# Kernel tuning notes

Measured on AMD Instinct MI355X. Metric: run time of the kernel, lower is better.

The kernel has to match this reference:

```python
import jax, jax.numpy as jnp
import numpy as np

B, L, D_MODEL = 2, 4096, 1024
D_INNER = 2048  # expand * d_model
D_CONV = 4


def setup_inputs() -> dict:
    key = jax.random.key(0)
    ks = jax.random.split(key, 7)
    return {
        "hidden_states": jax.random.normal(ks[0], (B, L, D_MODEL), jnp.float32),
        "W_in": jax.random.normal(ks[1], (2 * D_INNER, D_MODEL), jnp.float32) * 0.02,
        "conv_w": jax.random.normal(ks[2], (D_INNER, D_CONV), jnp.float32) * 0.1,
        "conv_b": jax.random.normal(ks[3], (D_INNER,), jnp.float32) * 0.1,
        "k_ssm": jax.random.normal(ks[4], (D_INNER, L), jnp.float32) * 0.02,  # materialized SSM kernel (channels=1)
        "D_skip": jax.random.normal(ks[5], (D_INNER,), jnp.float32),
        "W_out": jax.random.normal(ks[6], (D_MODEL, D_INNER), jnp.float32) * 0.02,
    }


def _silu(x):
    return x * jax.nn.sigmoid(x)


def reference(hidden_states, W_in, conv_w, conv_b, k_ssm, D_skip, W_out):
    Bq, Lq, _ = hidden_states.shape
    # in_proj (no bias): (B, L, d_model) -> (B, 2*d_inner, L)
    xz = jnp.einsum('bld,ed->bel', hidden_states, W_in)
    x, z = jnp.split(xz, 2, axis=1)  # each (B, d_inner, L)

    # causal depthwise conv1d (pad left d_conv-1) + SiLU (causal_conv1d_fn)
    xp = jnp.pad(x, ((0, 0), (0, 0), (D_CONV - 1, 0)))
    xc = conv_b[None, :, None]
    for j in range(D_CONV):
        xc = xc + conv_w[None, :, j, None] * xp[:, :, j:j + Lq]
    x = _silu(xc)

    # FFT long convolution (l_kernel = L, n = 2L), channels = 1
    n = 2 * Lq
    x_f = jnp.fft.rfft(x, n=n)            # (B, H, n//2+1) complex
    k_f = jnp.fft.rfft(k_ssm, n=n)        # (H, n//2+1)
    y = jnp.fft.irfft(x_f * k_f[None], n=n)[..., :Lq]  # (B, H, L)

    # D skip connection
    y = y + x * D_skip[None, :, None]

    # gating with SiLU(z)
    y = y * _silu(z)

    # out_proj (no bias): (B, H, L) -> (B, L, d_model)
    return jnp.einsum('bhl,dh->bld', y, W_out)
```

## Files before the change

kernel.cpp:

```cpp
#include <hip/hip_runtime.h>
#include <hip/hip_bf16.h>
#include <math.h>

#define B_SZ 2
#define L_SZ 4096
#define DM   1024
#define DI   2048
#define E_SZ 4096
#define DC   4

typedef unsigned short u16;
typedef __attribute__((ext_vector_type(8))) short short8;
typedef __attribute__((ext_vector_type(4))) float f32x4;

__device__ __forceinline__ float silu_f(float v) {
    return v / (1.0f + __expf(-v));
}

__device__ __forceinline__ void split_bf16(float x, u16& h, u16& l) {
    unsigned u  = __float_as_uint(x);
    unsigned hb = u & 0xFFFF0000u;
    h = (u16)(hb >> 16);
    float lf = x - __uint_as_float(hb);
    l = (u16)(__float_as_uint(lf) >> 16);
}
__device__ __forceinline__ float bf2f(u16 h) {
    return __uint_as_float(((unsigned)h) << 16);
}

__device__ __forceinline__ void gld_lds16(const u16* g, u16* l) {
    __builtin_amdgcn_global_load_lds(
        (const __attribute__((address_space(1))) unsigned int*)g,
        (__attribute__((address_space(3))) unsigned int*)l, 16, 0, 0);
}

__global__ __launch_bounds__(256) void pack_rm(
    const float* __restrict__ X, u16* __restrict__ H, u16* __restrict__ Lo,
    int ldx, int r16n, long sX, long sOut)
{
    const long cid = (long)blockIdx.x * 256 + threadIdx.x;
    const int  qc  = (int)(cid & 63);
    const long blk = cid >> 6;
    const int  r16 = (int)(blk % r16n);
    const int  k32 = (int)(blk / r16n);
    const int  q = qc >> 4, m = qc & 15;

    const float* src = X + blockIdx.y * sX + (long)(r16 * 16 + m) * ldx + k32 * 32 + q * 8;
    float4 v0 = *(const float4*)src;
    float4 v1 = *(const float4*)(src + 4);
    float v[8] = {v0.x,v0.y,v0.z,v0.w,v1.x,v1.y,v1.z,v1.w};

    u16 hs[8], ls[8];
    #pragma unroll
    for (int j = 0; j < 8; ++j) split_bf16(v[j], hs[j], ls[j]);

    const long o = blockIdx.y * sOut + cid * 8;
    *(uint4*)&H[o]  = *(const uint4*)hs;
    *(uint4*)&Lo[o] = *(const uint4*)ls;
}

__global__ __launch_bounds__(256) void gemm_mfma(
    const u16* __restrict__ Ah, const u16* __restrict__ Al,
    const u16* __restrict__ Bh, const u16* __restrict__ Bl,
    float* __restrict__ C,
    int r16A, int r16B, long sA, long sB, long sC,
    int ldc, int nk32)
{
    __shared__ alignas(16) u16 sm[4][4096];

    const int tid  = threadIdx.x;
    const int wv   = tid >> 6, lane = tid & 63;
    const long zb  = blockIdx.z;

    const u16* srcs0 = Ah + zb * sA;
    const u16* srcs1 = Al + zb * sA;
    const u16* srcs2 = Bh + zb * sB;
    const u16* srcs3 = Bl + zb * sB;
    const u16* mysrc = (wv == 0) ? srcs0 : (wv == 1) ? srcs1 : (wv == 2) ? srcs2 : srcs3;
    const int  rblk  = (wv < 2) ? blockIdx.x * 8 : blockIdx.y * 8;
    const int  r16c  = (wv < 2) ? r16A : r16B;
    u16* myl = sm[wv];

    const int wr = wv >> 1, wc = wv & 1;

    f32x4 acc[4][4];
    #pragma unroll
    for (int i = 0; i < 4; ++i)
        #pragma unroll
        for (int j = 0; j < 4; ++j)
            #pragma unroll
            for (int r = 0; r < 4; ++r) acc[i][j][r] = 0.f;

    for (int s = 0; s < nk32; ++s) {
        if (s) __syncthreads();
        {
            const u16* g = mysrc + (((long)s * r16c + rblk) << 9) + lane * 8;
            #pragma unroll
            for (int i = 0; i < 8; ++i)
                gld_lds16(g + (i << 9), myl + (i << 9));
        }
        __syncthreads();

        short8 afh[4], afl[4], bfh[4], bfl[4];
        const int aoff = (wr * 4) * 512 + lane * 8;
        const int boff = (wc * 4) * 512 + lane * 8;
        #pragma unroll
        for (int t = 0; t < 4; ++t) {
            afh[t] = *(const short8*)&sm[0][aoff + t * 512];
            afl[t] = *(const short8*)&sm[1][aoff + t * 512];
            bfh[t] = *(const short8*)&sm[2][boff + t * 512];
            bfl[t] = *(const short8*)&sm[3][boff + t * 512];
        }
        #pragma unroll
        for (int i = 0; i < 4; ++i)
            #pragma unroll
            for (int j = 0; j < 4; ++j) {
                acc[i][j] = __builtin_amdgcn_mfma_f32_16x16x32_bf16(afh[i], bfh[j], acc[i][j], 0, 0, 0);
                acc[i][j] = __builtin_amdgcn_mfma_f32_16x16x32_bf16(afh[i], bfl[j], acc[i][j], 0, 0, 0);
                acc[i][j] = __builtin_amdgcn_mfma_f32_16x16x32_bf16(afl[i], bfh[j], acc[i][j], 0, 0, 0);
            }
    }

    const int m_ = lane & 15, q_ = lane >> 4;
    float* Cb = C + zb * sC;
    const int row00 = blockIdx.x * 128 + wr * 64 + q_ * 4;
    const int col0  = blockIdx.y * 128 + wc * 64 + m_;
    #pragma unroll
    for (int i = 0; i < 4; ++i)
        #pragma unroll
        for (int j = 0; j < 4; ++j) {
            const long base = (long)(row00 + i * 16) * ldc + col0 + j * 16;
            #pragma unroll
            for (int r = 0; r < 4; ++r)
                Cb[base + (long)r * ldc] = acc[i][j][r];
        }
}

__global__ __launch_bounds__(256) void conv_silu_split(
    const float* __restrict__ xz, const float* __restrict__ conv_w,
    const float* __restrict__ conv_b,
    u16* __restrict__ xh_gl, u16* __restrict__ xl_gl)
{
    const long gid = (long)blockIdx.x * 256 + threadIdx.x;
    const int  q   = (int)(gid % (L_SZ / 4));
    const long bc  = gid / (L_SZ / 4);
    const int  ch  = (int)(bc % DI);
    const int  b   = (int)(bc / DI);

    const float* row = xz + ((long)b * E_SZ + ch) * L_SZ;
    const int l0 = q * 4;

    float4 cur  = *(const float4*)&row[l0];
    float4 prev = q ? *(const float4*)&row[l0 - 4] : make_float4(0.f, 0.f, 0.f, 0.f);

    const float w0 = conv_w[ch*DC+0], w1 = conv_w[ch*DC+1];
    const float w2 = conv_w[ch*DC+2], w3 = conv_w[ch*DC+3];
    const float bias = conv_b[ch];

    float o[4];
    o[0] = silu_f(bias + w0*prev.y + w1*prev.z + w2*prev.w + w3*cur.x);
    o[1] = silu_f(bias + w0*prev.z + w1*prev.w + w2*cur.x  + w3*cur.y);
    o[2] = silu_f(bias + w0*prev.w + w1*cur.x  + w2*cur.y  + w3*cur.z);
    o[3] = silu_f(bias + w0*cur.x  + w1*cur.y  + w2*cur.z  + w3*cur.w);

    unsigned long long hp = 0ull, lp = 0ull;
    #pragma unroll
    for (int r = 0; r < 4; ++r) {
        u16 h, l; split_bf16(o[r], h, l);
        hp |= ((unsigned long long)h) << (16*r);
        lp |= ((unsigned long long)l) << (16*r);
    }
    const long base = ((long)b * DI + ch) * L_SZ + l0;
    *(unsigned long long*)&xh_gl[base] = hp;
    *(unsigned long long*)&xl_gl[base] = lp;
}

__global__ __launch_bounds__(128, 2) void longconv_mfma(
    u16* __restrict__ xh_gl, u16* __restrict__ xl_gl,
    const float* __restrict__ xz,  const float* __restrict__ k_ssm,
    const float* __restrict__ D_skip)
{
    __shared__ u16 Xh[2][4352];
    __shared__ u16 Xl[2][4352];

    const int lane = threadIdx.x & 63;
    const int wv   = threadIdx.x >> 6;
    const int wc   = blockIdx.x * 2 + wv;
    const int ch   = wc & (DI - 1);
    const int b    = wc >> 11;

    u16*         xhr  = xh_gl + ((long)b * DI + ch) * L_SZ;
    u16*         xlr  = xl_gl + ((long)b * DI + ch) * L_SZ;
    const float* krow = k_ssm + (long)ch * L_SZ;

    u16* XH = Xh[wv];
    u16* XL = Xl[wv];

    if (lane < 32) {
        uint4 z = make_uint4(0u, 0u, 0u, 0u);
        *(uint4*)&XH[lane * 8] = z;
        *(uint4*)&XL[lane * 8] = z;
    }
    #pragma unroll
    for (int it = 0; it < 8; ++it) {
        const int idx = it * 64 + lane;
        *(uint4*)&XH[256 + idx * 8] = ((const uint4*)xhr)[idx];
        *(uint4*)&XL[256 + idx * 8] = ((const uint4*)xlr)[idx];
    }
    __syncthreads();

    const int m_ = lane & 15;
    const int q_ = lane >> 4;
    const int dq = m_ - 8 * q_ + ((q_ >= 2) ? 32 : 0);
    const int xoff_lane = 256 + 16 * m_ + 8 * q_ - ((q_ >= 2) ? 32 : 0);

    f32x4 acc[16];
    #pragma unroll
    for (int t = 0; t < 16; ++t)
        #pragma unroll
        for (int r = 0; r < 4; ++r) acc[t][r] = 0.f;

    float kn[8];
    #pragma unroll
    for (int e = 0; e < 8; ++e) {
        const int ki = dq - e;
        kn[e] = (ki >= 0) ? krow[ki] : 0.0f;
    }

    for (int c = 0; c < 128; ++c) {
        float kv[8];
        #pragma unroll
        for (int e = 0; e < 8; ++e) kv[e] = kn[e];
        if (c < 127) {
            #pragma unroll
            for (int e = 0; e < 8; ++e) {
                const int ki = 32 * (c + 1) + dq - e;
                kn[e] = (ki >= 0) ? krow[ki] : 0.0f;
            }
        }

        short8 ah, al;
        #pragma unroll
        for (int e = 0; e < 8; ++e) {
            u16 h, l; split_bf16(kv[e], h, l);
            ah[e] = (short)h; al[e] = (short)l;
        }

        const int xbase = xoff_lane - 32 * c;
        #pragma unroll
        for (int t = 0; t < 16; ++t) {
            if (8 * t >= c - 7) {
                short8 bh = *(const short8*)&XH[xbase + 256 * t];
                short8 bl = *(const short8*)&XL[xbase + 256 * t];
                acc[t] = __builtin_amdgcn_mfma_f32_16x16x32_bf16(ah, bh, acc[t], 0, 0, 0);
                acc[t] = __builtin_amdgcn_mfma_f32_16x16x32_bf16(ah, bl, acc[t], 0, 0, 0);
                acc[t] = __builtin_amdgcn_mfma_f32_16x16x32_bf16(al, bh, acc[t], 0, 0, 0);
            }
        }
    }

    const float  Ds   = D_skip[ch];
    const float* zrow = xz + ((long)b * E_SZ + DI + ch) * L_SZ;

    #pragma unroll
    for (int t = 0; t < 16; ++t) {
        const int l0 = 256 * t + 16 * m_ + 4 * q_;
        float4 zv = *(const float4*)&zrow[l0];
        float zt[4] = { zv.x, zv.y, zv.z, zv.w };
        unsigned long long hp = 0ull, lp = 0ull;
        #pragma unroll
        for (int r = 0; r < 4; ++r) {
            const float xf = bf2f(XH[256 + l0 + r]) + bf2f(XL[256 + l0 + r]);
            const float o  = (acc[t][r] + Ds * xf) * silu_f(zt[r]);
            u16 h, l; split_bf16(o, h, l);
            hp |= ((unsigned long long)h) << (16*r);
            lp |= ((unsigned long long)l) << (16*r);
        }
        *(unsigned long long*)&xhr[l0] = hp;
        *(unsigned long long*)&xlr[l0] = lp;
    }
}

__global__ __launch_bounds__(256) void pack_y(
    const u16* __restrict__ Yh, const u16* __restrict__ Yl,
    u16* __restrict__ OH, u16* __restrict__ OL, long sOut)
{
    __shared__ u16 T[2][32][136];
    const int t  = threadIdx.x;
    const int l0 = blockIdx.x * 128;
    const int h0 = blockIdx.y * 32;
    const int b  = blockIdx.z;

    const u16* yb_h = Yh + ((long)b * DI + h0) * L_SZ + l0;
    const u16* yb_l = Yl + ((long)b * DI + h0) * L_SZ + l0;

    #pragma unroll
    for (int i = 0; i < 2; ++i) {
        const int c = t + 256 * i;
        const int row = c >> 4, col = (c & 15) * 8;
        *(uint4*)&T[0][row][col] = *(const uint4*)&yb_h[(long)row * L_SZ + col];
        *(uint4*)&T[1][row][col] = *(const uint4*)&yb_l[(long)row * L_SZ + col];
    }
    __syncthreads();

    u16* outs[2] = { OH + b * sOut, OL + b * sOut };
    #pragma unroll
    for (int p = 0; p < 2; ++p) {
        #pragma unroll
        for (int i = 0; i < 2; ++i) {
            const int c = t + 256 * i;
            const int r16b = c >> 6, qc = c & 63;
            const int q = qc >> 4, m = qc & 15;
            const int l = r16b * 16 + m;
            u16 vals[8];
            #pragma unroll
            for (int j = 0; j < 8; ++j) vals[j] = T[p][q * 8 + j][l];
            const long o = ((long)(blockIdx.y * 256 + blockIdx.x * 8 + r16b) << 9) + qc * 8;
            *(uint4*)&outs[p][o] = *(const uint4*)vals;
        }
    }
}

extern "C" void kernel_launch(void* const* d_in, const int* in_sizes, int n_in,
                              void* d_out, int out_size, void* d_ws, size_t ws_size,
                              hipStream_t stream)
{
    const float* hidden = (const float*)d_in[0];
    const float* W_in   = (const float*)d_in[1];
    const float* conv_w = (const float*)d_in[2];
    const float* conv_b = (const float*)d_in[3];
    const float* k_ssm  = (const float*)d_in[4];
    const float* D_skip = (const float*)d_in[5];
    const float* W_out  = (const float*)d_in[6];
    float* out = (float*)d_out;

    char* ws = (char*)d_ws;
    float* xz  = (float*)ws;
    u16*   xh  = (u16*)(ws + 134217728);
    u16*   xl  = (u16*)(ws + 167772160);
    u16*   WinH  = (u16*)(ws + 201326592);
    u16*   WinL  = WinH + 4194304;
    u16*   WoutH = (u16*)(ws + 201326592);
    u16*   WoutL = WoutH + 2097152;
    u16*   hidH  = (u16*)(ws + 218103808);
    u16*   hidL  = hidH + 8388608;
    u16*   yAh   = (u16*)ws;
    u16*   yAl   = yAh + 8388608;

    pack_rm<<<dim3(2048, 1), 256, 0, stream>>>(W_in, WinH, WinL, DM, 256, 0L, 0L);
    pack_rm<<<dim3(2048, B_SZ), 256, 0, stream>>>(hidden, hidH, hidL, DM, 256,
        (long)L_SZ * DM, 4194304L);

    gemm_mfma<<<dim3(32, 32, B_SZ), 256, 0, stream>>>(
        WinH, WinL, hidH, hidL, xz,
        256, 256, 0L, 4194304L, (long)E_SZ * L_SZ, L_SZ, 32);

    conv_silu_split<<<dim3((unsigned)((long)B_SZ*DI*(L_SZ/4)/256)), 256, 0, stream>>>(
        xz, conv_w, conv_b, xh, xl);

    longconv_mfma<<<dim3((B_SZ * DI) / 2), 128, 0, stream>>>(
        xh, xl, xz, k_ssm, D_skip);

    pack_rm<<<dim3(1024, 1), 256, 0, stream>>>(W_out, WoutH, WoutL, DI, 64, 0L, 0L);

    pack_y<<<dim3(32, 64, B_SZ), 256, 0, stream>>>(
        xh, xl, yAh, yAl, 33554432L);

    gemm_mfma<<<dim3(32, 8, B_SZ), 256, 0, stream>>>(
        yAh, yAl, WoutH, WoutL, out,
        256, 64, 33554432L, 0L, (long)L_SZ * DM, DM, 64);
}
```

Measured before the change: 693.4 us.

## Split each channel's long convolution across four waves with balanced tile sets

The causal long-convolution kernel now gives each (batch, channel) row to one 256-thread block instead of one wave. Each of the four waves owns four output tiles, chosen in mirrored pairs (wv, 7-wv, 8+wv, 15-wv) so the triangular workload is balanced. Each wave also stops its k-chunk loop at its largest tile. This cuts per-wave accumulator registers from 16 tiles to 4 and raises parallelism and occupancy. In exchange, the four waves load the same k values redundantly and the per-block shared-memory footprint per channel changes.

```diff
diff --git a/kernel.cpp b/kernel.cpp
--- a/kernel.cpp
+++ b/kernel.cpp
@@ -175,17 +175,18 @@
     *(unsigned long long*)&xl_gl[base] = lp;
 }
 
-__global__ __launch_bounds__(128, 2) void longconv_mfma(
+__global__ __launch_bounds__(256, 4) void longconv_mfma(
     u16* __restrict__ xh_gl, u16* __restrict__ xl_gl,
     const float* __restrict__ xz,  const float* __restrict__ k_ssm,
     const float* __restrict__ D_skip)
 {
-    __shared__ u16 Xh[2][4352];
-    __shared__ u16 Xl[2][4352];
-
-    const int lane = threadIdx.x & 63;
-    const int wv   = threadIdx.x >> 6;
-    const int wc   = blockIdx.x * 2 + wv;
+    __shared__ u16 XH[4352];
+    __shared__ u16 XL[4352];
+
+    const int tid  = threadIdx.x;
+    const int lane = tid & 63;
+    const int wv   = tid >> 6;
+    const int wc   = blockIdx.x;
     const int ch   = wc & (DI - 1);
     const int b    = wc >> 11;
 
@@ -193,17 +194,13 @@
     u16*         xlr  = xl_gl + ((long)b * DI + ch) * L_SZ;
     const float* krow = k_ssm + (long)ch * L_SZ;
 
-    u16* XH = Xh[wv];
-    u16* XL = Xl[wv];
-
-    if (lane < 32) {
+    if (tid < 64) {
         uint4 z = make_uint4(0u, 0u, 0u, 0u);
-        *(uint4*)&XH[lane * 8] = z;
-        *(uint4*)&XL[lane * 8] = z;
-    }
-    #pragma unroll
-    for (int it = 0; it < 8; ++it) {
-        const int idx = it * 64 + lane;
+        ((uint4*)((tid < 32) ? XH : XL))[tid & 31] = z;
+    }
+    #pragma unroll
+    for (int it = 0; it < 2; ++it) {
+        const int idx = it * 256 + tid;
         *(uint4*)&XH[256 + idx * 8] = ((const uint4*)xhr)[idx];
         *(uint4*)&XL[256 + idx * 8] = ((const uint4*)xlr)[idx];
     }
@@ -214,11 +211,15 @@
     const int dq = m_ - 8 * q_ + ((q_ >= 2) ? 32 : 0);
     const int xoff_lane = 256 + 16 * m_ + 8 * q_ - ((q_ >= 2) ? 32 : 0);
 
-    f32x4 acc[16];
-    #pragma unroll
-    for (int t = 0; t < 16; ++t)
-        #pragma unroll
-        for (int r = 0; r < 4; ++r) acc[t][r] = 0.f;
+    const int tset[4] = { wv, 7 - wv, 8 + wv, 15 - wv };
+    const int tmax = 15 - wv;
+    const int cmax = 8 * tmax + 7;
+
+    f32x4 acc[4];
+    #pragma unroll
+    for (int u = 0; u < 4; ++u)
+        #pragma unroll
+        for (int r = 0; r < 4; ++r) acc[u][r] = 0.f;
 
     float kn[8];
     #pragma unroll
@@ -227,11 +228,11 @@
         kn[e] = (ki >= 0) ? krow[ki] : 0.0f;
     }
 
-    for (int c = 0; c < 128; ++c) {
+    for (int c = 0; c <= cmax; ++c) {
         float kv[8];
         #pragma unroll
         for (int e = 0; e < 8; ++e) kv[e] = kn[e];
-        if (c < 127) {
+        if (c < cmax) {
             #pragma unroll
             for (int e = 0; e < 8; ++e) {
                 const int ki = 32 * (c + 1) + dq - e;
@@ -248,13 +249,14 @@
 
         const int xbase = xoff_lane - 32 * c;
         #pragma unroll
-        for (int t = 0; t < 16; ++t) {
+        for (int u = 0; u < 4; ++u) {
+            const int t = tset[u];
             if (8 * t >= c - 7) {
                 short8 bh = *(const short8*)&XH[xbase + 256 * t];
                 short8 bl = *(const short8*)&XL[xbase + 256 * t];
-                acc[t] = __builtin_amdgcn_mfma_f32_16x16x32_bf16(ah, bh, acc[t], 0, 0, 0);
-                acc[t] = __builtin_amdgcn_mfma_f32_16x16x32_bf16(ah, bl, acc[t], 0, 0, 0);
-                acc[t] = __builtin_amdgcn_mfma_f32_16x16x32_bf16(al, bh, acc[t], 0, 0, 0);
+                acc[u] = __builtin_amdgcn_mfma_f32_16x16x32_bf16(ah, bh, acc[u], 0, 0, 0);
+                acc[u] = __builtin_amdgcn_mfma_f32_16x16x32_bf16(ah, bl, acc[u], 0, 0, 0);
+                acc[u] = __builtin_amdgcn_mfma_f32_16x16x32_bf16(al, bh, acc[u], 0, 0, 0);
             }
         }
     }
@@ -263,7 +265,8 @@
     const float* zrow = xz + ((long)b * E_SZ + DI + ch) * L_SZ;
 
     #pragma unroll
-    for (int t = 0; t < 16; ++t) {
+    for (int u = 0; u < 4; ++u) {
+        const int t  = tset[u];
         const int l0 = 256 * t + 16 * m_ + 4 * q_;
         float4 zv = *(const float4*)&zrow[l0];
         float zt[4] = { zv.x, zv.y, zv.z, zv.w };
@@ -271,7 +274,7 @@
         #pragma unroll
         for (int r = 0; r < 4; ++r) {
             const float xf = bf2f(XH[256 + l0 + r]) + bf2f(XL[256 + l0 + r]);
-            const float o  = (acc[t][r] + Ds * xf) * silu_f(zt[r]);
+            const float o  = (acc[u][r] + Ds * xf) * silu_f(zt[r]);
             u16 h, l; split_bf16(o, h, l);
             hp |= ((unsigned long long)h) << (16*r);
             lp |= ((unsigned long long)l) << (16*r);
@@ -358,7 +361,7 @@
     conv_silu_split<<<dim3((unsigned)((long)B_SZ*DI*(L_SZ/4)/256)), 256, 0, stream>>>(
         xz, conv_w, conv_b, xh, xl);
 
-    longconv_mfma<<<dim3((B_SZ * DI) / 2), 128, 0, stream>>>(
+    longconv_mfma<<<dim3(B_SZ * DI), 256, 0, stream>>>(
         xh, xl, xz, k_ssm, D_skip);
 
     pack_rm<<<dim3(1024, 1), 256, 0, stream>>>(W_out, WoutH, WoutL, DI, 64, 0L, 0L);
```

New measurement: 635.3 us. 8.4% less time.
